# Kernel tuning notes

Hardware: AMD Instinct MI355X
Metric: run time of the kernel (lower is better)

The kernel has to match this reference:

```python
import jax, jax.numpy as jnp
import numpy as np

NUM_USERS = 100000
NUM_ITEMS = 50000
N = NUM_USERS + NUM_ITEMS  # total nodes
DIM = 64                   # dim_h
E = 2000000                # number of edges
NUM_LAYERS = 2


def setup_inputs() -> dict:
    key = jax.random.key(0)
    k0, k1, k2, k3, k4 = jax.random.split(key, 5)
    edge_index = jax.random.randint(k0, (2, E), 0, N, dtype=jnp.int64)
    edge_weight = jax.random.uniform(k1, (E,), dtype=jnp.float32)
    # nn.init.normal_(std=0.01) embeddings
    emb_users = 0.01 * jax.random.normal(k2, (NUM_USERS, DIM), dtype=jnp.float32)
    emb_items = 0.01 * jax.random.normal(k3, (NUM_ITEMS, DIM), dtype=jnp.float32)
    # nn.Linear(dim_h, dim_h)
    kW, kb = jax.random.split(k4)
    bound = 1.0 / np.sqrt(DIM)
    W = jax.random.uniform(kW, (DIM, DIM), minval=-bound, maxval=bound, dtype=jnp.float32)
    b = jax.random.uniform(kb, (DIM,), minval=-bound, maxval=bound, dtype=jnp.float32)
    return {"edge_index": edge_index, "edge_weight": edge_weight,
            "emb_users": emb_users, "emb_items": emb_items, "W": W, "b": b}


def reference(edge_index, edge_weight, emb_users, emb_items, W, b):
    # emb = cat([user_emb, item_emb])  -> [N, DIM]
    emb = jnp.concatenate([emb_users, emb_items], axis=0)
    src, dst = edge_index[0], edge_index[1]
    acc = emb  # running sum over layer embeddings (embs list)
    for _ in range(NUM_LAYERS):
        # LGConv with edge_weight: out[i] = sum_{j->i} w * x[j], then .relu()
        msg = edge_weight[:, None] * emb[src]            # [E, DIM] gather
        emb = jax.nn.relu(jax.ops.segment_sum(msg, dst, num_segments=N))
        acc = acc + emb
    emb_final = acc / (NUM_LAYERS + 1)                   # mean over stacked embs
    emb_final = emb_final @ W.T + b                      # final linear
    emb_users_final = emb_final[:NUM_USERS]
    emb_items_final = emb_final[NUM_USERS:]
    return (emb_users_final, emb_users, emb_items_final, emb_items)
```

## Files before the change

### kernel.cpp

```cpp
#include <hip/hip_runtime.h>
#include <hip/hip_fp16.h>

#define NUSERS 100000
#define NITEMS 50000
#define NNODES (NUSERS + NITEMS)
#define DIM 64
#define NEDGE 2000000

#define BSH 7
#define NB ((NNODES + 127) >> BSH)
#define CAP 2048
#define CHUNK 4096
#define ABLOCKS ((NEDGE + CHUNK - 1) / CHUNK)
#define CONVB ((NNODES * DIM / 4 + 511) / 512)

#define NTILES (NNODES / 16)
#define FTB ((NTILES + 7) / 8)

typedef _Float16 f16x8 __attribute__((ext_vector_type(8)));
typedef float f32x4 __attribute__((ext_vector_type(4)));

__global__ __launch_bounds__(512)
void bucketconv_kernel(const int* __restrict__ eidx, const float* __restrict__ ew,
                       int* __restrict__ gcur, int2* __restrict__ regions,
                       const float* __restrict__ eu, const float* __restrict__ eit,
                       __half* __restrict__ tbl, float* __restrict__ out) {
    const int t = threadIdx.x;

    if (blockIdx.x >= ABLOCKS) {
        long i = (long)(blockIdx.x - ABLOCKS) * 512 + t;
        const long total = (long)NNODES * DIM / 4;
        if (i < total) {
            const long ue = (long)NUSERS * DIM / 4;
            float4 v;
            if (i < ue) {
                v = ((const float4*)eu)[i];
                ((float4*)(out + (long)NUSERS * DIM))[i] = v;
            } else {
                long j = i - ue;
                v = ((const float4*)eit)[j];
                ((float4*)(out + (long)2 * NUSERS * DIM + (long)NITEMS * DIM))[j] = v;
            }
            ((__half2*)tbl)[2 * i + 0] = __floats2half2_rn(v.x, v.y);
            ((__half2*)tbl)[2 * i + 1] = __floats2half2_rn(v.z, v.w);
        }
        return;
    }

    __shared__ int cursor_s[NB];
    __shared__ int excl_s[NB];
    __shared__ int gbase_s[NB];
    __shared__ int scanbuf[512];
    __shared__ int2 stage[CHUNK];
    __shared__ unsigned short sbkt[CHUNK];

    const int e0 = blockIdx.x * CHUNK;
    const int cnt_edges = min(CHUNK, NEDGE - e0);

    for (int i = t; i < NB; i += 512) cursor_s[i] = 0;
    __syncthreads();

    int2 recs[8];
    int bk[8];
    const int e4base = e0 >> 2;
#pragma unroll
    for (int k = 0; k < 2; ++k) {
        int g = k * 512 + t;
        bool ok = (4 * g) < cnt_edges;
        int4 s4 = make_int4(0, 0, 0, 0), d4 = make_int4(0, 0, 0, 0);
        float4 w4 = make_float4(0.f, 0.f, 0.f, 0.f);
        if (ok) {
            int e4 = e4base + g;
            s4 = ((const int4*)eidx)[e4];
            d4 = ((const int4*)eidx)[(NEDGE >> 2) + e4];
            w4 = ((const float4*)ew)[e4];
        }
        int ss[4] = {s4.x, s4.y, s4.z, s4.w};
        int dd[4] = {d4.x, d4.y, d4.z, d4.w};
        float ww[4] = {w4.x, w4.y, w4.z, w4.w};
#pragma unroll
        for (int j = 0; j < 4; ++j) {
            int idx = 4 * k + j;
            if (ok) {
                int d = dd[j];
                int b = d >> BSH;
                bk[idx] = b;
                recs[idx].x = ss[j] | ((d & 127) << 18);
                recs[idx].y = __float_as_int(ww[j]);
                atomicAdd(&cursor_s[b], 1);
            } else {
                bk[idx] = -1;
            }
        }
    }
    __syncthreads();

    int myv[3];
    int tsum = 0;
    const int base_i = t * 3;
#pragma unroll
    for (int j = 0; j < 3; ++j) {
        int i = base_i + j;
        myv[j] = (i < NB) ? cursor_s[i] : 0;
        tsum += myv[j];
    }
    scanbuf[t] = tsum;
    __syncthreads();
    for (int d = 1; d < 512; d <<= 1) {
        int u = (t >= d) ? scanbuf[t - d] : 0;
        __syncthreads();
        scanbuf[t] += u;
        __syncthreads();
    }
    int run = scanbuf[t] - tsum;
#pragma unroll
    for (int j = 0; j < 3; ++j) {
        int i = base_i + j;
        if (i < NB) {
            excl_s[i] = run;
            cursor_s[i] = run;
            if (myv[j] > 0) gbase_s[i] = atomicAdd(&gcur[i], myv[j]);
            run += myv[j];
        }
    }
    __syncthreads();

#pragma unroll
    for (int k = 0; k < 8; ++k) {
        if (bk[k] >= 0) {
            int p = atomicAdd(&cursor_s[bk[k]], 1);
            stage[p] = recs[k];
            sbkt[p] = (unsigned short)bk[k];
        }
    }
    __syncthreads();

    for (int i = t; i < cnt_edges; i += 512) {
        int b = sbkt[i];
        int gpos = gbase_s[b] + (i - excl_s[b]);
        if (gpos < CAP) regions[(long)b * CAP + gpos] = stage[i];
    }
}

__global__ __launch_bounds__(512)
void sortpull1_kernel(const int* __restrict__ gcur, const int2* __restrict__ regions,
                      const __half* __restrict__ tbl,
                      int2* __restrict__ edge_sorted, int2* __restrict__ rs,
                      __half* __restrict__ buf1h) {
    __shared__ int2 srec[CAP];
    __shared__ int cnt[128];
    __shared__ int excl[128];
    __shared__ int scanbuf[128];
    const int t = threadIdx.x;
    const int b = blockIdx.x;
    const int node0 = b << BSH;
    const int ecnt = min(gcur[b], CAP);
    const long gbase = (long)b * CAP;

    if (t < 128) cnt[t] = 0;
    __syncthreads();

    int2 recs[4];
#pragma unroll
    for (int k = 0; k < 4; ++k) {
        int i = k * 512 + t;
        if (i < ecnt) {
            recs[k] = regions[gbase + i];
            atomicAdd(&cnt[(recs[k].x >> 18) & 127], 1);
        }
    }
    __syncthreads();

    if (t < 128) scanbuf[t] = cnt[t];
    __syncthreads();
    for (int d = 1; d < 128; d <<= 1) {
        int u = 0;
        if (t < 128 && t >= d) u = scanbuf[t - d];
        __syncthreads();
        if (t < 128) scanbuf[t] += u;
        __syncthreads();
    }
    if (t < 128) {
        excl[t] = scanbuf[t] - cnt[t];
        cnt[t] = scanbuf[t] - cnt[t];
    }
    __syncthreads();

#pragma unroll
    for (int k = 0; k < 4; ++k) {
        int i = k * 512 + t;
        if (i < ecnt) {
            int d = (recs[k].x >> 18) & 127;
            int p = atomicAdd(&cnt[d], 1);
            int2 o;
            o.x = recs[k].x & 0x3FFFF;
            o.y = recs[k].y;
            srec[p] = o;
        }
    }
    __syncthreads();

    for (int i = t; i < ecnt; i += 512) edge_sorted[gbase + i] = srec[i];
    if (t < 128) {
        int node = node0 + t;
        if (node < NNODES) {
            int2 p;
            p.x = (int)gbase + excl[t];
            p.y = (int)gbase + cnt[t];
            rs[node] = p;
        }
    }

    const int lane = t & 63;
    const int wv = t >> 6;
    const int g = lane >> 4;
    const int gl = lane & 15;
    const int2* tb4 = (const int2*)tbl;
#pragma unroll 1
    for (int j = 0; j < 16; ++j) {
        const int local = wv * 16 + j;
        const int node = node0 + local;
        if (node >= NNODES) break;
        int i = excl[local];
        const int iend = cnt[local];
        float4 acc = make_float4(0.f, 0.f, 0.f, 0.f);
        for (; i + 15 < iend; i += 16) {
#pragma unroll
            for (int u = 0; u < 4; ++u) {
                int2 r = srec[i + 4 * u + g];
                float w = __int_as_float(r.y);
                int2 hv = tb4[((long)r.x << 4) + gl];
                float2 f0 = __half22float2(*(const __half2*)&hv.x);
                float2 f1 = __half22float2(*(const __half2*)&hv.y);
                acc.x = fmaf(w, f0.x, acc.x); acc.y = fmaf(w, f0.y, acc.y);
                acc.z = fmaf(w, f1.x, acc.z); acc.w = fmaf(w, f1.y, acc.w);
            }
        }
        if (i < iend) {
#pragma unroll
            for (int u = 0; u < 4; ++u) {
                int idx = i + 4 * u + g;
                if (idx < iend) {
                    int2 r = srec[idx];
                    float w = __int_as_float(r.y);
                    int2 hv = tb4[((long)r.x << 4) + gl];
                    float2 f0 = __half22float2(*(const __half2*)&hv.x);
                    float2 f1 = __half22float2(*(const __half2*)&hv.y);
                    acc.x = fmaf(w, f0.x, acc.x); acc.y = fmaf(w, f0.y, acc.y);
                    acc.z = fmaf(w, f1.x, acc.z); acc.w = fmaf(w, f1.y, acc.w);
                }
            }
        }
        acc.x += __shfl_xor(acc.x, 16); acc.y += __shfl_xor(acc.y, 16);
        acc.z += __shfl_xor(acc.z, 16); acc.w += __shfl_xor(acc.w, 16);
        acc.x += __shfl_xor(acc.x, 32); acc.y += __shfl_xor(acc.y, 32);
        acc.z += __shfl_xor(acc.z, 32); acc.w += __shfl_xor(acc.w, 32);
        if (g == 0) {
            __half2 o0 = __floats2half2_rn(fmaxf(acc.x, 0.f), fmaxf(acc.y, 0.f));
            __half2 o1 = __floats2half2_rn(fmaxf(acc.z, 0.f), fmaxf(acc.w, 0.f));
            int2 ov;
            ov.x = *(const int*)&o0;
            ov.y = *(const int*)&o1;
            ((int2*)buf1h)[((long)node << 4) + gl] = ov;
        }
    }
}

__global__ __launch_bounds__(512)
void pull2_kernel(const int* __restrict__ gcur, const int2* __restrict__ rs,
                  const int2* __restrict__ edge_sorted,
                  const __half* __restrict__ in_emb,
                  __half* __restrict__ out_emb) {
    __shared__ int2 srec[CAP];
    __shared__ int2 rsl[128];
    const int t = threadIdx.x;
    const int b = blockIdx.x;
    const int node0 = b << BSH;
    const int ecnt = min(gcur[b], CAP);
    const long gbase = (long)b * CAP;

    for (int i = t; i < ecnt; i += 512) srec[i] = edge_sorted[gbase + i];
    if (t < 128) {
        int node = node0 + t;
        rsl[t] = (node < NNODES) ? rs[node] : make_int2(0, 0);
    }
    __syncthreads();

    const int lane = t & 63;
    const int wv = t >> 6;
    const int g = lane >> 4;
    const int gl = lane & 15;
    const int2* tb4 = (const int2*)in_emb;
#pragma unroll 1
    for (int j = 0; j < 16; ++j) {
        const int local = wv * 16 + j;
        const int node = node0 + local;
        if (node >= NNODES) break;
        int i = rsl[local].x - (int)gbase;
        const int iend = rsl[local].y - (int)gbase;
        float4 acc = make_float4(0.f, 0.f, 0.f, 0.f);
        for (; i + 15 < iend; i += 16) {
#pragma unroll
            for (int u = 0; u < 4; ++u) {
                int2 r = srec[i + 4 * u + g];
                float w = __int_as_float(r.y);
                int2 hv = tb4[((long)r.x << 4) + gl];
                float2 f0 = __half22float2(*(const __half2*)&hv.x);
                float2 f1 = __half22float2(*(const __half2*)&hv.y);
                acc.x = fmaf(w, f0.x, acc.x); acc.y = fmaf(w, f0.y, acc.y);
                acc.z = fmaf(w, f1.x, acc.z); acc.w = fmaf(w, f1.y, acc.w);
            }
        }
        if (i < iend) {
#pragma unroll
            for (int u = 0; u < 4; ++u) {
                int idx = i + 4 * u + g;
                if (idx < iend) {
                    int2 r = srec[idx];
                    float w = __int_as_float(r.y);
                    int2 hv = tb4[((long)r.x << 4) + gl];
                    float2 f0 = __half22float2(*(const __half2*)&hv.x);
                    float2 f1 = __half22float2(*(const __half2*)&hv.y);
                    acc.x = fmaf(w, f0.x, acc.x); acc.y = fmaf(w, f0.y, acc.y);
                    acc.z = fmaf(w, f1.x, acc.z); acc.w = fmaf(w, f1.y, acc.w);
                }
            }
        }
        acc.x += __shfl_xor(acc.x, 16); acc.y += __shfl_xor(acc.y, 16);
        acc.z += __shfl_xor(acc.z, 16); acc.w += __shfl_xor(acc.w, 16);
        acc.x += __shfl_xor(acc.x, 32); acc.y += __shfl_xor(acc.y, 32);
        acc.z += __shfl_xor(acc.z, 32); acc.w += __shfl_xor(acc.w, 32);
        if (g == 0) {
            __half2 o0 = __floats2half2_rn(fmaxf(acc.x, 0.f), fmaxf(acc.y, 0.f));
            __half2 o1 = __floats2half2_rn(fmaxf(acc.z, 0.f), fmaxf(acc.w, 0.f));
            int2 ov;
            ov.x = *(const int*)&o0;
            ov.y = *(const int*)&o1;
            ((int2*)out_emb)[((long)node << 4) + gl] = ov;
        }
    }
}

__global__ __launch_bounds__(512)
void final_kernel(const __half* __restrict__ tbl, const __half* __restrict__ e1,
                  const __half* __restrict__ e2, const float* __restrict__ W,
                  const float* __restrict__ bias, float* __restrict__ out) {
    const int t = threadIdx.x;
    const int lane = t & 63;
    const int wv = t >> 6;
    const int tile = blockIdx.x * 8 + wv;
    if (tile >= NTILES) return;
    const int m = lane & 15;
    const int kg = lane >> 4;

    f16x8 bfr[4][2];
#pragma unroll
    for (int nt = 0; nt < 4; ++nt) {
#pragma unroll
        for (int kh = 0; kh < 2; ++kh) {
            const float4* wp = (const float4*)(W + (nt * 16 + m) * 64 + kh * 32 + kg * 8);
            float4 w0 = wp[0], w1 = wp[1];
            f16x8 bb;
            bb[0] = (_Float16)w0.x; bb[1] = (_Float16)w0.y;
            bb[2] = (_Float16)w0.z; bb[3] = (_Float16)w0.w;
            bb[4] = (_Float16)w1.x; bb[5] = (_Float16)w1.y;
            bb[6] = (_Float16)w1.z; bb[7] = (_Float16)w1.w;
            bfr[nt][kh] = bb;
        }
    }
    float bs[4];
#pragma unroll
    for (int nt = 0; nt < 4; ++nt) bs[nt] = bias[nt * 16 + m];

    const long rowA = (long)tile * 16 + m;
    f16x8 afr[2];
#pragma unroll
    for (int kh = 0; kh < 2; ++kh) {
        long off = rowA * 64 + kh * 32 + kg * 8;
        f16x8 a0 = *(const f16x8*)(tbl + off);
        f16x8 a1 = *(const f16x8*)(e1 + off);
        f16x8 a2 = *(const f16x8*)(e2 + off);
        afr[kh] = a0 + a1 + a2;
    }

    f32x4 acc[4];
#pragma unroll
    for (int nt = 0; nt < 4; ++nt) {
        acc[nt] = (f32x4){0.f, 0.f, 0.f, 0.f};
        acc[nt] = __builtin_amdgcn_mfma_f32_16x16x32_f16(afr[0], bfr[nt][0], acc[nt], 0, 0, 0);
        acc[nt] = __builtin_amdgcn_mfma_f32_16x16x32_f16(afr[1], bfr[nt][1], acc[nt], 0, 0, 0);
    }

#pragma unroll
    for (int r = 0; r < 4; ++r) {
        long row = (long)tile * 16 + kg * 4 + r;
        long o = (row < NUSERS) ? row * DIM
                                : (long)2 * NUSERS * DIM + (row - NUSERS) * DIM;
#pragma unroll
        for (int nt = 0; nt < 4; ++nt) {
            out[o + nt * 16 + m] = fmaf(acc[nt][r], (1.0f / 3.0f), bs[nt]);
        }
    }
}

extern "C" void kernel_launch(void* const* d_in, const int* in_sizes, int n_in,
                              void* d_out, int out_size, void* d_ws, size_t ws_size,
                              hipStream_t stream) {
    const int*   eidx = (const int*)d_in[0];
    const float* ew   = (const float*)d_in[1];
    const float* eu   = (const float*)d_in[2];
    const float* eit  = (const float*)d_in[3];
    const float* W    = (const float*)d_in[4];
    const float* bias = (const float*)d_in[5];
    float* out = (float*)d_out;

    const size_t nfeat = (size_t)NNODES * DIM;
    __half* tbl         = (__half*)d_ws;
    __half* buf1h       = tbl + nfeat;
    __half* buf2h       = buf1h + nfeat;
    int2*   regions     = (int2*)(buf2h + nfeat);
    int2*   edge_sorted = regions + (long)NB * CAP;
    int2*   rs          = edge_sorted + (long)NB * CAP;
    int*    gcur        = (int*)(rs + NNODES);

    hipMemsetAsync(gcur, 0, NB * sizeof(int), stream);

    bucketconv_kernel<<<ABLOCKS + CONVB, 512, 0, stream>>>(eidx, ew, gcur, regions,
                                                           eu, eit, tbl, out);

    sortpull1_kernel<<<NB, 512, 0, stream>>>(gcur, regions, tbl,
                                             edge_sorted, rs, buf1h);

    pull2_kernel<<<NB, 512, 0, stream>>>(gcur, rs, edge_sorted, buf1h, buf2h);

    final_kernel<<<FTB, 512, 0, stream>>>(tbl, buf1h, buf2h, W, bias, out);
}
```

Measured before the change: 312.0 us.

## Fuse second propagation layer with final linear projection via LDS staging

Result: faster. 296.9 us (-4.8%).

```diff
diff --git a/kernel.cpp b/kernel.cpp
--- a/kernel.cpp
+++ b/kernel.cpp
@@ -13,9 +13,6 @@
 #define CHUNK 4096
 #define ABLOCKS ((NEDGE + CHUNK - 1) / CHUNK)
 #define CONVB ((NNODES * DIM / 4 + 511) / 512)
-
-#define NTILES (NNODES / 16)
-#define FTB ((NTILES + 7) / 8)
 
 typedef _Float16 f16x8 __attribute__((ext_vector_type(8)));
 typedef float f32x4 __attribute__((ext_vector_type(4)));
@@ -267,12 +264,15 @@
 }
 
 __global__ __launch_bounds__(512)
-void pull2_kernel(const int* __restrict__ gcur, const int2* __restrict__ rs,
-                  const int2* __restrict__ edge_sorted,
-                  const __half* __restrict__ in_emb,
-                  __half* __restrict__ out_emb) {
+void pull2final_kernel(const int* __restrict__ gcur, const int2* __restrict__ rs,
+                       const int2* __restrict__ edge_sorted,
+                       const __half* __restrict__ buf1h,
+                       const __half* __restrict__ tbl,
+                       const float* __restrict__ W, const float* __restrict__ bias,
+                       float* __restrict__ out) {
     __shared__ int2 srec[CAP];
     __shared__ int2 rsl[128];
+    __shared__ __half e2t[128][72];
     const int t = threadIdx.x;
     const int b = blockIdx.x;
     const int node0 = b << BSH;
@@ -290,7 +290,7 @@
     const int wv = t >> 6;
     const int g = lane >> 4;
     const int gl = lane & 15;
-    const int2* tb4 = (const int2*)in_emb;
+    const int2* tb4 = (const int2*)buf1h;
 #pragma unroll 1
     for (int j = 0; j < 16; ++j) {
         const int local = wv * 16 + j;
@@ -336,20 +336,11 @@
             int2 ov;
             ov.x = *(const int*)&o0;
             ov.y = *(const int*)&o1;
-            ((int2*)out_emb)[((long)node << 4) + gl] = ov;
-        }
-    }
-}
-
-__global__ __launch_bounds__(512)
-void final_kernel(const __half* __restrict__ tbl, const __half* __restrict__ e1,
-                  const __half* __restrict__ e2, const float* __restrict__ W,
-                  const float* __restrict__ bias, float* __restrict__ out) {
-    const int t = threadIdx.x;
-    const int lane = t & 63;
-    const int wv = t >> 6;
-    const int tile = blockIdx.x * 8 + wv;
-    if (tile >= NTILES) return;
+            *(int2*)(&e2t[local][gl << 2]) = ov;
+        }
+    }
+
+    if (node0 + wv * 16 >= NNODES) return;
     const int m = lane & 15;
     const int kg = lane >> 4;
 
@@ -372,33 +363,34 @@
 #pragma unroll
     for (int nt = 0; nt < 4; ++nt) bs[nt] = bias[nt * 16 + m];
 
-    const long rowA = (long)tile * 16 + m;
+    const int lr = wv * 16 + m;
+    const long rowA = (long)node0 + lr;
     f16x8 afr[2];
 #pragma unroll
     for (int kh = 0; kh < 2; ++kh) {
         long off = rowA * 64 + kh * 32 + kg * 8;
         f16x8 a0 = *(const f16x8*)(tbl + off);
-        f16x8 a1 = *(const f16x8*)(e1 + off);
-        f16x8 a2 = *(const f16x8*)(e2 + off);
+        f16x8 a1 = *(const f16x8*)(buf1h + off);
+        f16x8 a2 = *(const f16x8*)(&e2t[lr][kh * 32 + kg * 8]);
         afr[kh] = a0 + a1 + a2;
     }
 
-    f32x4 acc[4];
+    f32x4 accd[4];
 #pragma unroll
     for (int nt = 0; nt < 4; ++nt) {
-        acc[nt] = (f32x4){0.f, 0.f, 0.f, 0.f};
-        acc[nt] = __builtin_amdgcn_mfma_f32_16x16x32_f16(afr[0], bfr[nt][0], acc[nt], 0, 0, 0);
-        acc[nt] = __builtin_amdgcn_mfma_f32_16x16x32_f16(afr[1], bfr[nt][1], acc[nt], 0, 0, 0);
+        accd[nt] = (f32x4){0.f, 0.f, 0.f, 0.f};
+        accd[nt] = __builtin_amdgcn_mfma_f32_16x16x32_f16(afr[0], bfr[nt][0], accd[nt], 0, 0, 0);
+        accd[nt] = __builtin_amdgcn_mfma_f32_16x16x32_f16(afr[1], bfr[nt][1], accd[nt], 0, 0, 0);
     }
 
 #pragma unroll
     for (int r = 0; r < 4; ++r) {
-        long row = (long)tile * 16 + kg * 4 + r;
+        long row = (long)node0 + wv * 16 + kg * 4 + r;
         long o = (row < NUSERS) ? row * DIM
                                 : (long)2 * NUSERS * DIM + (row - NUSERS) * DIM;
 #pragma unroll
         for (int nt = 0; nt < 4; ++nt) {
-            out[o + nt * 16 + m] = fmaf(acc[nt][r], (1.0f / 3.0f), bs[nt]);
+            out[o + nt * 16 + m] = fmaf(accd[nt][r], (1.0f / 3.0f), bs[nt]);
         }
     }
 }
@@ -417,8 +409,7 @@
     const size_t nfeat = (size_t)NNODES * DIM;
     __half* tbl         = (__half*)d_ws;
     __half* buf1h       = tbl + nfeat;
-    __half* buf2h       = buf1h + nfeat;
-    int2*   regions     = (int2*)(buf2h + nfeat);
+    int2*   regions     = (int2*)(buf1h + nfeat);
     int2*   edge_sorted = regions + (long)NB * CAP;
     int2*   rs          = edge_sorted + (long)NB * CAP;
     int*    gcur        = (int*)(rs + NNODES);
@@ -431,7 +422,6 @@
     sortpull1_kernel<<<NB, 512, 0, stream>>>(gcur, regions, tbl,
                                              edge_sorted, rs, buf1h);
 
-    pull2_kernel<<<NB, 512, 0, stream>>>(gcur, rs, edge_sorted, buf1h, buf2h);
-
-    final_kernel<<<FTB, 512, 0, stream>>>(tbl, buf1h, buf2h, W, bias, out);
+    pull2final_kernel<<<NB, 512, 0, stream>>>(gcur, rs, edge_sorted, buf1h,
+                                              tbl, W, bias, out);
 }
```
